# Performance work log

Measured on AMD Instinct MI355X. Metric: run time of the kernel, lower is better.

Reference implementation:

```python
import jax, jax.numpy as jnp
import numpy as np
from jax.scipy.linalg import cho_solve

N_OBS = 2_000_000
DIM = 16
EPS = 1e-6
LOG_DIM = 32  # module uses self.dim = 32 (param count) in the log-2pi term; faithful to source


def _block_diag_cov(params):
    # params: (32,) -> 8 blocks of 2x2, block = B @ B^T + eps*I, assembled block-diagonally
    B = params.reshape(8, 2, 2)
    blocks = jnp.einsum('nij,nkj->nik', B, B) + EPS * jnp.eye(2, dtype=params.dtype)
    idx = jnp.arange(8)
    M = jnp.zeros((8, 2, 8, 2), dtype=params.dtype).at[idx, :, idx, :].set(blocks)
    return M.reshape(16, 16)


def _transform_mu(mu, pose):
    # interleaved (x,y) points, rotate about centroid, translate to pose[:2]
    pts = jnp.stack([mu[0::2], mu[1::2]])  # (2, 8)
    centroid = jnp.mean(pts, axis=1, keepdims=True)
    ct, st = jnp.cos(pose[2]), jnp.sin(pose[2])
    R = jnp.stack([jnp.stack([ct, -st]), jnp.stack([st, ct])])  # (2,2)
    pts = R @ (pts - centroid) + pose[:2, None]
    return jnp.zeros(16, dtype=mu.dtype).at[0::2].set(pts[0]).at[1::2].set(pts[1])


def setup_inputs() -> dict:
    key = jax.random.key(0)
    k1, k2, k3, k4, k5 = jax.random.split(key, 5)
    obs = jax.random.normal(k1, (N_OBS, DIM), dtype=jnp.float32)
    mu_likelihood = jax.random.normal(k2, (DIM,), dtype=jnp.float32)
    # pose init ~ [uniform(15,25), uniform(15,25), uniform(-pi/16, pi/16)]
    u = jax.random.uniform(k3, (3,), dtype=jnp.float32)
    mu_prior_pose = jnp.array([15.0, 15.0, -np.pi / 16], jnp.float32) + u * jnp.array([10.0, 10.0, 2 * np.pi / 16], jnp.float32)
    # covariance params ~ uniform(cov_min=0.01, cov_max=10)
    Sigma_prior_params = jax.random.uniform(k4, (32,), dtype=jnp.float32, minval=0.01, maxval=10.0)
    Sigma_likelihood_params = jax.random.uniform(k5, (32,), dtype=jnp.float32, minval=0.01, maxval=10.0)
    return {
        'obs': obs,
        'mu_likelihood': mu_likelihood,
        'mu_prior_pose': mu_prior_pose,
        'Sigma_prior_params': Sigma_prior_params,
        'Sigma_likelihood_params': Sigma_likelihood_params,
    }


def reference(obs, mu_likelihood, mu_prior_pose, Sigma_prior_params, Sigma_likelihood_params):
    Sigma_prior = _block_diag_cov(Sigma_prior_params)
    Sigma_likelihood = _block_diag_cov(Sigma_likelihood_params)
    eye = jnp.eye(DIM, dtype=jnp.float32)

    L_prior = jnp.linalg.cholesky(Sigma_prior)
    prior_precision = cho_solve((L_prior, True), eye)
    L_like = jnp.linalg.cholesky(Sigma_likelihood)
    like_precision = cho_solve((L_like, True), eye)

    posterior_precision = prior_precision + like_precision
    L_post = jnp.linalg.cholesky(posterior_precision)
    Sigma_post = cho_solve((L_post, True), eye)

    mu_prior = _transform_mu(mu_likelihood, mu_prior_pose)
    mu_post = Sigma_post @ (cho_solve((L_prior, True), mu_prior) + cho_solve((L_like, True), mu_likelihood))

    diff = obs - mu_post  # (N, 16)
    # NOTE: faithful to source, which uses logdet of the *precision* and
    # quad form with Sigma_post = inv(posterior_precision)
    logdet = 2.0 * jnp.sum(jnp.log(jnp.diagonal(L_post)))
    quad = jnp.sum((diff @ Sigma_post) * diff, axis=1)  # (N,)
    log_terms = -0.5 * LOG_DIM * jnp.log(jnp.asarray(2.0 * jnp.pi, jnp.float32)) - 0.5 * logdet - 0.5 * quad
    return -jnp.sum(log_terms)
```

## Files before the change

### kernel.cpp

```cpp
#include <hip/hip_runtime.h>
#include <math.h>

#define EPS_COV 1e-6


__global__ void setup_kernel(const float* __restrict__ mu_like,
                             const float* __restrict__ pose,
                             const float* __restrict__ sp_prior,
                             const float* __restrict__ sp_like,
                             double* __restrict__ wsd,
                             float* __restrict__ setup)
{
    if (blockIdx.x != 0 || threadIdx.x != 0) return;
    wsd[0] = 0.0;

    double cx = 0.0, cy = 0.0;
    for (int i = 0; i < 8; ++i) { cx += (double)mu_like[2*i]; cy += (double)mu_like[2*i+1]; }
    cx *= 0.125; cy *= 0.125;
    double th = (double)pose[2], ct = cos(th), st = sin(th);
    double tx = (double)pose[0], ty = (double)pose[1];

    double logdet = 0.0;
    for (int n = 0; n < 8; ++n) {
        double px = (double)mu_like[2*n]   - cx;
        double py = (double)mu_like[2*n+1] - cy;
        double mp0 = ct*px - st*py + tx;
        double mp1 = st*px + ct*py + ty;

        const float* p = sp_prior + 4*n;
        double s00 = (double)p[0]*p[0] + (double)p[1]*p[1] + EPS_COV;
        double s01 = (double)p[0]*p[2] + (double)p[1]*p[3];
        double s11 = (double)p[2]*p[2] + (double)p[3]*p[3] + EPS_COV;
        double det = s00*s11 - s01*s01;
        double Pp00 = s11/det, Pp01 = -s01/det, Pp11 = s00/det;

        const float* l = sp_like + 4*n;
        double t00 = (double)l[0]*l[0] + (double)l[1]*l[1] + EPS_COV;
        double t01 = (double)l[0]*l[2] + (double)l[1]*l[3];
        double t11 = (double)l[2]*l[2] + (double)l[3]*l[3] + EPS_COV;
        double dl = t00*t11 - t01*t01;
        double Pl00 = t11/dl, Pl01 = -t01/dl, Pl11 = t00/dl;

        double Q00 = Pp00 + Pl00, Q01 = Pp01 + Pl01, Q11 = Pp11 + Pl11;
        double dq = Q00*Q11 - Q01*Q01;
        logdet += log(dq);
        double S00 = Q11/dq, S01 = -Q01/dq, S11v = Q00/dq;

        double ml0 = (double)mu_like[2*n], ml1 = (double)mu_like[2*n+1];
        double v0 = Pp00*mp0 + Pp01*mp1 + Pl00*ml0 + Pl01*ml1;
        double v1 = Pp01*mp0 + Pp11*mp1 + Pl01*ml0 + Pl11*ml1;
        setup[2*n]   = (float)(S00*v0 + S01*v1);
        setup[2*n+1] = (float)(S01*v0 + S11v*v1);

        setup[16+n] = (float)S00;
        setup[24+n] = (float)(2.0*S01);
        setup[32+n] = (float)S11v;
    }
    wsd[1] = logdet;
}

__global__ __launch_bounds__(256) void quad_kernel(
    const float4* __restrict__ obs4,
    const float*  __restrict__ setup,
    double* __restrict__ acc,
    int n4)
{
    const int tid    = blockIdx.x * blockDim.x + threadIdx.x;
    const int stride = gridDim.x * blockDim.x;
    const int q = tid & 3;

    const float m0 = setup[4*q+0], m1 = setup[4*q+1];
    const float m2 = setup[4*q+2], m3 = setup[4*q+3];
    const float a0 = setup[16+2*q],   b0 = setup[24+2*q],   c0 = setup[32+2*q];
    const float a1 = setup[16+2*q+1], b1 = setup[24+2*q+1], c1 = setup[32+2*q+1];

    double accd = 0.0;
    #pragma unroll 4
    for (int i = tid; i < n4; i += stride) {
        float4 v = obs4[i];
        float d0 = v.x - m0, d1 = v.y - m1;
        float d2 = v.z - m2, d3 = v.w - m3;
        float pq = a0*d0*d0 + b0*d0*d1 + c0*d1*d1
                 + a1*d2*d2 + b1*d2*d3 + c1*d3*d3;
        accd += (double)pq;
    }

    #pragma unroll
    for (int off = 32; off > 0; off >>= 1)
        accd += __shfl_down(accd, off, 64);

    __shared__ double lds[4];
    const int wave = threadIdx.x >> 6;
    if ((threadIdx.x & 63) == 0) lds[wave] = accd;
    __syncthreads();
    if (threadIdx.x == 0) {
        double s = lds[0] + lds[1] + lds[2] + lds[3];
        atomicAdd(acc, s);
    }
}

__global__ void finalize_kernel(const double* __restrict__ wsd,
                                float* __restrict__ out,
                                double n_obs)
{
    if (blockIdx.x != 0 || threadIdx.x != 0) return;
    const double LOG_2PI = 1.8378770664093454835606594728112;
    double c = n_obs * (16.0 * LOG_2PI + 0.5 * wsd[1]);
    out[0] = (float)(c + 0.5 * wsd[0]);
}

extern "C" void kernel_launch(void* const* d_in, const int* in_sizes, int n_in,
                              void* d_out, int out_size, void* d_ws, size_t ws_size,
                              hipStream_t stream) {
    const float* obs      = (const float*)d_in[0];
    const float* mu_like  = (const float*)d_in[1];
    const float* pose     = (const float*)d_in[2];
    const float* sp_prior = (const float*)d_in[3];
    const float* sp_like  = (const float*)d_in[4];
    float* out = (float*)d_out;

    double* wsd  = (double*)d_ws;
    float* setup = (float*)((char*)d_ws + 2 * sizeof(double));

    const int n_elems = in_sizes[0];
    const int n4      = n_elems / 4;
    const double n_obs = (double)(n_elems / 16);

    setup_kernel<<<1, 64, 0, stream>>>(mu_like, pose, sp_prior, sp_like, wsd, setup);

    const int threads = 256;
    const int blocks  = 2048;
    quad_kernel<<<blocks, threads, 0, stream>>>((const float4*)obs, setup, wsd, n4);

    finalize_kernel<<<1, 64, 0, stream>>>(wsd, out, n_obs);
}
```

Before: 204.0 us.

## Fuse setup and finalize into the streaming reduction kernel with last-block completion

Each thread now recomputes the tiny per-block 2x2 posterior parameters in fp32 instead of reading them from a separate single-thread setup kernel. The final scalar is written by the last block to finish, detected through an atomic counter, so the finalize kernel goes away. A memset replaces the in-kernel zeroing of the accumulator. This removes two kernel launches and their serial dependency, at the cost of redundant per-thread setup math and lower precision (float instead of double) in the posterior parameters and logdet.

```diff
diff --git a/kernel.cpp b/kernel.cpp
--- a/kernel.cpp
+++ b/kernel.cpp
@@ -1,78 +1,71 @@
 #include <hip/hip_runtime.h>
 #include <math.h>
 
-#define EPS_COV 1e-6
+#define EPS_COV 1e-6f
 
 
-__global__ void setup_kernel(const float* __restrict__ mu_like,
-                             const float* __restrict__ pose,
-                             const float* __restrict__ sp_prior,
-                             const float* __restrict__ sp_like,
-                             double* __restrict__ wsd,
-                             float* __restrict__ setup)
-{
-    if (blockIdx.x != 0 || threadIdx.x != 0) return;
-    wsd[0] = 0.0;
-
-    double cx = 0.0, cy = 0.0;
-    for (int i = 0; i < 8; ++i) { cx += (double)mu_like[2*i]; cy += (double)mu_like[2*i+1]; }
-    cx *= 0.125; cy *= 0.125;
-    double th = (double)pose[2], ct = cos(th), st = sin(th);
-    double tx = (double)pose[0], ty = (double)pose[1];
-
-    double logdet = 0.0;
-    for (int n = 0; n < 8; ++n) {
-        double px = (double)mu_like[2*n]   - cx;
-        double py = (double)mu_like[2*n+1] - cy;
-        double mp0 = ct*px - st*py + tx;
-        double mp1 = st*px + ct*py + ty;
-
-        const float* p = sp_prior + 4*n;
-        double s00 = (double)p[0]*p[0] + (double)p[1]*p[1] + EPS_COV;
-        double s01 = (double)p[0]*p[2] + (double)p[1]*p[3];
-        double s11 = (double)p[2]*p[2] + (double)p[3]*p[3] + EPS_COV;
-        double det = s00*s11 - s01*s01;
-        double Pp00 = s11/det, Pp01 = -s01/det, Pp11 = s00/det;
-
-        const float* l = sp_like + 4*n;
-        double t00 = (double)l[0]*l[0] + (double)l[1]*l[1] + EPS_COV;
-        double t01 = (double)l[0]*l[2] + (double)l[1]*l[3];
-        double t11 = (double)l[2]*l[2] + (double)l[3]*l[3] + EPS_COV;
-        double dl = t00*t11 - t01*t01;
-        double Pl00 = t11/dl, Pl01 = -t01/dl, Pl11 = t00/dl;
-
-        double Q00 = Pp00 + Pl00, Q01 = Pp01 + Pl01, Q11 = Pp11 + Pl11;
-        double dq = Q00*Q11 - Q01*Q01;
-        logdet += log(dq);
-        double S00 = Q11/dq, S01 = -Q01/dq, S11v = Q00/dq;
-
-        double ml0 = (double)mu_like[2*n], ml1 = (double)mu_like[2*n+1];
-        double v0 = Pp00*mp0 + Pp01*mp1 + Pl00*ml0 + Pl01*ml1;
-        double v1 = Pp01*mp0 + Pp11*mp1 + Pl01*ml0 + Pl11*ml1;
-        setup[2*n]   = (float)(S00*v0 + S01*v1);
-        setup[2*n+1] = (float)(S01*v0 + S11v*v1);
-
-        setup[16+n] = (float)S00;
-        setup[24+n] = (float)(2.0*S01);
-        setup[32+n] = (float)S11v;
-    }
-    wsd[1] = logdet;
-}
-
-__global__ __launch_bounds__(256) void quad_kernel(
+__global__ __launch_bounds__(256) void bayes_fused_kernel(
     const float4* __restrict__ obs4,
-    const float*  __restrict__ setup,
-    double* __restrict__ acc,
-    int n4)
+    const float*  __restrict__ mu_like,
+    const float*  __restrict__ pose,
+    const float*  __restrict__ sp_prior,
+    const float*  __restrict__ sp_like,
+    double*       __restrict__ acc,
+    unsigned int* __restrict__ ctr,
+    float*        __restrict__ out,
+    int n4, double n_obs)
 {
     const int tid    = blockIdx.x * blockDim.x + threadIdx.x;
     const int stride = gridDim.x * blockDim.x;
     const int q = tid & 3;
 
-    const float m0 = setup[4*q+0], m1 = setup[4*q+1];
-    const float m2 = setup[4*q+2], m3 = setup[4*q+3];
-    const float a0 = setup[16+2*q],   b0 = setup[24+2*q],   c0 = setup[32+2*q];
-    const float a1 = setup[16+2*q+1], b1 = setup[24+2*q+1], c1 = setup[32+2*q+1];
+    float cx = 0.f, cy = 0.f;
+    #pragma unroll
+    for (int i = 0; i < 8; ++i) { cx += mu_like[2*i]; cy += mu_like[2*i+1]; }
+    cx *= 0.125f; cy *= 0.125f;
+    const float th = pose[2];
+    const float ct = cosf(th), st = sinf(th);
+    const float tx = pose[0], ty = pose[1];
+
+    float m0=0.f, m1=0.f, m2=0.f, m3=0.f;
+    float a0=0.f, b0=0.f, c0=0.f, a1=0.f, b1=0.f, c1=0.f;
+    float logdet = 0.f;
+
+    #pragma unroll
+    for (int n = 0; n < 8; ++n) {
+        float px = mu_like[2*n]   - cx;
+        float py = mu_like[2*n+1] - cy;
+        float mp0 = ct*px - st*py + tx;
+        float mp1 = st*px + ct*py + ty;
+
+        const float* p = sp_prior + 4*n;
+        float s00 = p[0]*p[0] + p[1]*p[1] + EPS_COV;
+        float s01 = p[0]*p[2] + p[1]*p[3];
+        float s11 = p[2]*p[2] + p[3]*p[3] + EPS_COV;
+        float det = s00*s11 - s01*s01;
+        float Pp00 =  s11/det, Pp01 = -s01/det, Pp11 = s00/det;
+
+        const float* l = sp_like + 4*n;
+        float t00 = l[0]*l[0] + l[1]*l[1] + EPS_COV;
+        float t01 = l[0]*l[2] + l[1]*l[3];
+        float t11 = l[2]*l[2] + l[3]*l[3] + EPS_COV;
+        float dl = t00*t11 - t01*t01;
+        float Pl00 =  t11/dl, Pl01 = -t01/dl, Pl11 = t00/dl;
+
+        float Q00 = Pp00 + Pl00, Q01 = Pp01 + Pl01, Q11 = Pp11 + Pl11;
+        float dq = Q00*Q11 - Q01*Q01;
+        logdet += logf(dq);
+        float S00 = Q11/dq, S01 = -Q01/dq, S11v = Q00/dq;
+
+        float ml0 = mu_like[2*n], ml1 = mu_like[2*n+1];
+        float v0 = Pp00*mp0 + Pp01*mp1 + Pl00*ml0 + Pl01*ml1;
+        float v1 = Pp01*mp0 + Pp11*mp1 + Pl01*ml0 + Pl11*ml1;
+        float mpostx = S00*v0 + S01*v1;
+        float mposty = S01*v0 + S11v*v1;
+
+        if (n == 2*q)     { m0 = mpostx; m1 = mposty; a0 = S00; b0 = 2.f*S01; c0 = S11v; }
+        if (n == 2*q + 1) { m2 = mpostx; m3 = mposty; a1 = S00; b1 = 2.f*S01; c1 = S11v; }
+    }
 
     double accd = 0.0;
     #pragma unroll 4
@@ -93,20 +86,19 @@
     const int wave = threadIdx.x >> 6;
     if ((threadIdx.x & 63) == 0) lds[wave] = accd;
     __syncthreads();
+
     if (threadIdx.x == 0) {
         double s = lds[0] + lds[1] + lds[2] + lds[3];
         atomicAdd(acc, s);
+        __threadfence();
+        unsigned int old = atomicAdd(ctr, 1u);
+        if (old == gridDim.x - 1) {
+            double total = atomicAdd(acc, 0.0);
+            const double LOG_2PI = 1.8378770664093454835606594728112;
+            double c = n_obs * (16.0 * LOG_2PI + 0.5 * (double)logdet);
+            out[0] = (float)(c + 0.5 * total);
+        }
     }
-}
-
-__global__ void finalize_kernel(const double* __restrict__ wsd,
-                                float* __restrict__ out,
-                                double n_obs)
-{
-    if (blockIdx.x != 0 || threadIdx.x != 0) return;
-    const double LOG_2PI = 1.8378770664093454835606594728112;
-    double c = n_obs * (16.0 * LOG_2PI + 0.5 * wsd[1]);
-    out[0] = (float)(c + 0.5 * wsd[0]);
 }
 
 extern "C" void kernel_launch(void* const* d_in, const int* in_sizes, int n_in,
@@ -119,18 +111,18 @@
     const float* sp_like  = (const float*)d_in[4];
     float* out = (float*)d_out;
 
-    double* wsd  = (double*)d_ws;
-    float* setup = (float*)((char*)d_ws + 2 * sizeof(double));
+    double*       acc = (double*)d_ws;
+    unsigned int* ctr = (unsigned int*)((char*)d_ws + 8);
 
-    const int n_elems = in_sizes[0];
-    const int n4      = n_elems / 4;
+    const int n_elems  = in_sizes[0];
+    const int n4       = n_elems / 4;
     const double n_obs = (double)(n_elems / 16);
 
-    setup_kernel<<<1, 64, 0, stream>>>(mu_like, pose, sp_prior, sp_like, wsd, setup);
+    hipMemsetAsync(d_ws, 0, 16, stream);
 
     const int threads = 256;
     const int blocks  = 2048;
-    quad_kernel<<<blocks, threads, 0, stream>>>((const float4*)obs, setup, wsd, n4);
-
-    finalize_kernel<<<1, 64, 0, stream>>>(wsd, out, n_obs);
+    bayes_fused_kernel<<<blocks, threads, 0, stream>>>(
+        (const float4*)obs, mu_like, pose, sp_prior, sp_like,
+        acc, ctr, out, n4, n_obs);
 }
```

After: 285.2 us. 1.4x slower.
